# Optimization experiments

Hardware: AMD Instinct MI355X
Metric: run time of the kernel (lower is better)

Reference implementation:

```python
import jax, jax.numpy as jnp
import numpy as np

N_HEAD = 20
ALIGN_HEAD_IDX = (4, 7, 11)  # heads of alignment_heads with layer_idx == layer_index (2)


def setup_inputs() -> dict:
    key = jax.random.key(0)
    ks = jax.random.split(key, 7)
    B, Tq, Tk, D = 8, 448, 1500, 1280
    s = 1.0 / np.sqrt(D)
    return {
        "x": jax.random.normal(ks[0], (B, Tq, D), jnp.float32),
        "k": jax.random.normal(ks[1], (B, Tk, D), jnp.float32),
        "v": jax.random.normal(ks[2], (B, Tk, D), jnp.float32),
        "Wq": jax.random.normal(ks[3], (D, D), jnp.float32) * s,
        "bq": jax.random.normal(ks[4], (D,), jnp.float32) * 0.02,
        "Wo": jax.random.normal(ks[5], (D, D), jnp.float32) * s,
        "bo": jax.random.normal(ks[6], (D,), jnp.float32) * 0.02,
    }


def reference(x, k, v, Wq, bq, Wo, bo):
    B, Tq, D = x.shape
    H = N_HEAD
    Dh = D // H
    scale = Dh ** (-0.25)

    # q projection (torch Linear: x @ W.T + b)
    q = x @ Wq.T + bq                                   # [B, Tq, D]
    qh = q.reshape(B, Tq, H, Dh).transpose(0, 2, 1, 3)  # [B, H, Tq, Dh]
    kh = k.reshape(B, -1, H, Dh).transpose(0, 2, 1, 3)  # [B, H, Tk, Dh]
    vh = v.reshape(B, -1, H, Dh).transpose(0, 2, 1, 3)  # [B, H, Tk, Dh]

    # scaled QK^T, softmax in fp32
    qk = jnp.einsum("bhqd,bhkd->bhqk", qh * scale, kh * scale)
    w = jax.nn.softmax(qk.astype(jnp.float32), axis=-1).astype(q.dtype)

    out = jnp.einsum("bhqk,bhkd->bhqd", w, vh)          # [B, H, Tq, Dh]
    out = out.transpose(0, 2, 1, 3).reshape(B, Tq, D)
    out = out @ Wo.T + bo

    alignment_weights = w[:, jnp.array(ALIGN_HEAD_IDX), :, :]  # [B, 3, Tq, Tk]
    return out, alignment_weights
```

## Files before the change

kernel.cpp:

```cpp
#include <hip/hip_runtime.h>
#include <stdint.h>


typedef short bf16x8 __attribute__((ext_vector_type(8)));
typedef float f32x4  __attribute__((ext_vector_type(4)));

#define VMCNT(n) asm volatile("s_waitcnt vmcnt(" #n ")" ::: "memory")

__device__ __forceinline__ unsigned short f2bf(float f) {
  union { float f; unsigned int u; } c; c.f = f;
  unsigned int u = c.u;
  unsigned int r = (u + 0x7FFFu + ((u >> 16) & 1u)) >> 16;
  return (unsigned short)r;
}

__device__ __forceinline__ float exp2_hw(float x) {
  float r;
  asm("v_exp_f32 %0, %1" : "=v"(r) : "v"(x));
  return r;
}

__device__ __forceinline__ void gld_lds16(const void* g, void* l) {
  __builtin_amdgcn_global_load_lds(
      (__attribute__((address_space(1))) void*)g,
      (__attribute__((address_space(3))) void*)l, 16, 0, 0);
}

__device__ __forceinline__ bf16x8 ldfrag(const void* base, int row, int c16) {
  return *reinterpret_cast<const bf16x8*>(
      reinterpret_cast<const char*>(base) + (row << 7) + (((c16 ^ (row & 7))) << 4));
}
__device__ __forceinline__ bf16x8 ldfragV(const void* base, int row, int c16) {
  return *reinterpret_cast<const bf16x8*>(
      reinterpret_cast<const char*>(base) + (row << 8) + (((c16 ^ (row & 15))) << 4));
}

__global__ __launch_bounds__(256) void prep_kernel(
    const float* __restrict__ x,  unsigned short* __restrict__ xb,
    const float* __restrict__ Wq, unsigned short* __restrict__ wqb,
    const float* __restrict__ Wo, unsigned short* __restrict__ wob,
    const float* __restrict__ k,  unsigned short* __restrict__ kb,
    const float* __restrict__ v,  unsigned short* __restrict__ vbt) {
  __shared__ float T[64][65];
  int blk = blockIdx.x;
  if (blk < 22680) {
    const float* src; unsigned short* dst;
    if (blk < 4480)       { src = x;  dst = xb; }
    else if (blk < 6080)  { src = Wq; dst = wqb; blk -= 4480; }
    else if (blk < 7680)  { src = Wo; dst = wob; blk -= 6080; }
    else                  { src = k;  dst = kb;  blk -= 7680; }
    long i = ((long)blk * 256 + threadIdx.x) * 4;
    float4 val = *reinterpret_cast<const float4*>(src + i);
    ushort4 o;
    o.x = f2bf(val.x); o.y = f2bf(val.y); o.z = f2bf(val.z); o.w = f2bf(val.w);
    *reinterpret_cast<ushort4*>(dst + i) = o;
    return;
  }
  blk -= 22680;
  const int kt = blk % 24; blk /= 24;
  const int h = blk % 20; const int b = blk / 20;
  const int tid = threadIdx.x;
  const int c  = tid & 63;
  const int r0 = tid >> 6;
#pragma unroll
  for (int r = 0; r < 16; ++r) {
    const int tk = r * 4 + r0;
    const int gtk = kt * 64 + tk;
    float val = 0.f;
    if (gtk < 1500) val = v[(size_t)(b * 1500 + gtk) * 1280 + h * 64 + c];
    T[tk][c] = val;
  }
  __syncthreads();
#pragma unroll
  for (int r = 0; r < 16; ++r) {
    const int d = r * 4 + r0;
    vbt[((size_t)(b * 20 + h) * 64 + d) * 1536 + kt * 64 + c] = f2bf(T[c][d]);
  }
}

template <int EPI>
__global__ __launch_bounds__(256) void gemm_bt(const unsigned short* __restrict__ A,
                                               const unsigned short* __restrict__ Bm,
                                               const float* __restrict__ bias,
                                               void* __restrict__ Cout,
                                               int M, int N, int K, float scale) {
  __shared__ __attribute__((aligned(16))) unsigned short As[128 * 64];
  __shared__ __attribute__((aligned(16))) unsigned short Bs[128 * 64];
  const int tid = threadIdx.x;
  const int w = tid >> 6, lane = tid & 63;
  const int l15 = lane & 15, l4 = lane >> 4;
  const int nBlk = N >> 7;
  const int cpx = gridDim.x >> 3;
  const int bid = (blockIdx.x & 7) * cpx + (blockIdx.x >> 3);
  const int bm = bid / nBlk, bn = bid % nBlk;
  const int m0 = bm << 7, n0 = bn << 7;
  const int wr = (w >> 1) << 6, wc = (w & 1) << 6;

  f32x4 acc[4][4] = {};

  const int nKt = K >> 6;
  for (int kt = 0; kt < nKt; ++kt) {
    const int koff = kt << 6;
#pragma unroll
    for (int r = 0; r < 4; ++r) {
      const int base = (((w << 2) + r) << 10);
      const int p = base + (lane << 4);
      const int row = p >> 7;
      const int cb = (p & 127) >> 1;
      gld_lds16(A  + ((size_t)(m0 + row) * K + koff + cb), (char*)As + base);
      gld_lds16(Bm + ((size_t)(n0 + row) * K + koff + cb), (char*)Bs + base);
    }
    __syncthreads();
#pragma unroll
    for (int kk = 0; kk < 64; kk += 32) {
      bf16x8 af[4], bfr[4];
#pragma unroll
      for (int mi = 0; mi < 4; ++mi)
        af[mi] = *reinterpret_cast<const bf16x8*>(&As[(wr + mi * 16 + l15) * 64 + kk + l4 * 8]);
#pragma unroll
      for (int ni = 0; ni < 4; ++ni)
        bfr[ni] = *reinterpret_cast<const bf16x8*>(&Bs[(wc + ni * 16 + l15) * 64 + kk + l4 * 8]);
#pragma unroll
      for (int mi = 0; mi < 4; ++mi)
#pragma unroll
        for (int ni = 0; ni < 4; ++ni)
          acc[mi][ni] = __builtin_amdgcn_mfma_f32_16x16x32_bf16(af[mi], bfr[ni], acc[mi][ni], 0, 0, 0);
    }
    __syncthreads();
  }
#pragma unroll
  for (int ni = 0; ni < 4; ++ni) {
    const int n = n0 + wc + ni * 16 + l15;
    const float bv = bias[n];
#pragma unroll
    for (int mi = 0; mi < 4; ++mi) {
#pragma unroll
      for (int i = 0; i < 4; ++i) {
        const int m = m0 + wr + mi * 16 + l4 * 4 + i;
        float vv = (acc[mi][ni][i] + bv) * scale;
        if (EPI == 0)
          ((unsigned short*)Cout)[(size_t)m * N + n] = f2bf(vv);
        else
          ((float*)Cout)[(size_t)m * N + n] = vv;
      }
    }
  }
}

__global__ __launch_bounds__(256, 2) void attn_kernel(const unsigned short* __restrict__ Qg,
                                                      const unsigned short* __restrict__ Kg,
                                                      const unsigned short* __restrict__ Vtg,
                                                      unsigned short* __restrict__ Og,
                                                      float* __restrict__ ML) {
  __shared__ __attribute__((aligned(16))) char smem[81920];
  char* const K0 = smem;
  char* const K1 = smem + 16384;
  char* const V0 = smem + 32768;
  char* const V1 = smem + 49152;
  char* const Pw = smem + 65536 + (threadIdx.x >> 6) * 4096;

  const int tid = threadIdx.x;
  const int w = tid >> 6, lane = tid & 63;
  const int l15 = lane & 15, l4 = lane >> 4;
  int bid = (blockIdx.x & 7) * 140 + (blockIdx.x >> 3);
  const int qt = bid % 7; bid /= 7;
  const int h = bid % 20; const int b = bid / 20;
  const int tq0 = qt << 6;

  const int srK = lane >> 3;
  const int scK = ((lane & 7) ^ srK) << 3;
  const int vr4 = lane >> 4;
  const size_t vbase = ((size_t)(b * 20 + h)) * 64 * 1536;

  bf16x8 qreg[4][2];
#pragma unroll
  for (int qg = 0; qg < 4; ++qg) {
    const unsigned short* qp =
        Qg + (size_t)(b * 448 + tq0 + qg * 16 + l15) * 1280 + h * 64 + l4 * 8;
    qreg[qg][0] = *reinterpret_cast<const bf16x8*>(qp);
    qreg[qg][1] = *reinterpret_cast<const bf16x8*>(qp + 32);
  }

  auto stage = [&](int k0, char* Kd, char* Vd) {
#pragma unroll
    for (int c = 0; c < 4; ++c) {
      const int ch = (w << 2) + c;
      int tk = k0 + ch * 8 + srK; if (tk > 1499) tk = 1499;
      gld_lds16(Kg + ((size_t)(b * 1500 + tk)) * 1280 + h * 64 + scK, Kd + ch * 1024);
    }
#pragma unroll
    for (int c = 0; c < 4; ++c) {
      const int ch = (w << 2) + c;
      const int d = (ch << 2) + vr4;
      const int col = ((lane & 15) ^ ((c << 2) + vr4)) << 3;
      gld_lds16(Vtg + vbase + (size_t)d * 1536 + k0 + col, Vd + ch * 1024);
    }
  };

  stage(0, K0, V0);
  VMCNT(0);
  __builtin_amdgcn_s_barrier();

  float l_p[4] = {0.f, 0.f, 0.f, 0.f};
  f32x4 o_acc[4][4] = {};

  for (int kt = 0; kt < 12; ++kt) {
    const int cur = kt & 1;
    const char* Kb = cur ? K1 : K0;
    const char* Vb = cur ? V1 : V0;

    if (kt < 11) {
      stage((kt + 1) << 7, cur ? K0 : K1, cur ? V0 : V1);
      VMCNT(8);
    } else {
      VMCNT(0);
    }
    __builtin_amdgcn_s_barrier();

    f32x4 s[2][4] = {};
    __builtin_amdgcn_s_setprio(1);
#pragma unroll
    for (int h2 = 0; h2 < 2; ++h2) {
      bf16x8 kf0 = ldfrag(Kb, (w << 5) + l15,      (h2 << 2) + l4);
      bf16x8 kf1 = ldfrag(Kb, (w << 5) + 16 + l15, (h2 << 2) + l4);
#pragma unroll
      for (int qg = 0; qg < 4; ++qg)
        s[0][qg] = __builtin_amdgcn_mfma_f32_16x16x32_bf16(kf0, qreg[qg][h2], s[0][qg], 0, 0, 0);
#pragma unroll
      for (int qg = 0; qg < 4; ++qg)
        s[1][qg] = __builtin_amdgcn_mfma_f32_16x16x32_bf16(kf1, qreg[qg][h2], s[1][qg], 0, 0, 0);
    }
    __builtin_amdgcn_s_setprio(0);

    if (kt == 11) {
#pragma unroll
      for (int kg = 0; kg < 2; ++kg)
#pragma unroll
        for (int i = 0; i < 4; ++i)
          if ((w << 5) + (kg << 4) + (l4 << 2) + i >= 92) {
#pragma unroll
            for (int qg = 0; qg < 4; ++qg) s[kg][qg][i] = -1e30f;
          }
    }

#pragma unroll
    for (int kg = 0; kg < 2; ++kg)
#pragma unroll
      for (int qg = 0; qg < 4; ++qg) {
#pragma unroll
        for (int i = 0; i < 4; ++i) {
          float e = exp2_hw(fmaf(s[kg][qg][i], 1.44269504f, -17.31234049f));
          s[kg][qg][i] = e;
          l_p[qg] += e;
        }
        unsigned int u0, u1;
        asm("v_cvt_pk_bf16_f32 %0, %1, %2" : "=v"(u0) : "v"(s[kg][qg][0]), "v"(s[kg][qg][1]));
        asm("v_cvt_pk_bf16_f32 %0, %1, %2" : "=v"(u1) : "v"(s[kg][qg][2]), "v"(s[kg][qg][3]));
        unsigned long long u01 = ((unsigned long long)u1 << 32) | u0;
        *reinterpret_cast<unsigned long long*>(
            Pw + (qg << 10) + (((kg << 1) + (l4 >> 1)) << 8) + (l15 << 4) + ((l4 & 1) << 3)) = u01;
      }

    __builtin_amdgcn_s_setprio(1);
    bf16x8 bv[4];
#pragma unroll
    for (int dg = 0; dg < 4; ++dg)
      bv[dg] = ldfragV(Vb, (dg << 4) + l15, (w << 2) + l4);
#pragma unroll
    for (int qg = 0; qg < 4; ++qg) {
      bf16x8 ap = *reinterpret_cast<const bf16x8*>(Pw + (qg << 10) + (lane << 4));
#pragma unroll
      for (int dg = 0; dg < 4; ++dg)
        o_acc[qg][dg] = __builtin_amdgcn_mfma_f32_16x16x32_bf16(ap, bv[dg], o_acc[qg][dg], 0, 0, 0);
    }
    __builtin_amdgcn_s_setprio(0);
    __builtin_amdgcn_s_barrier();
  }

#pragma unroll
  for (int qg = 0; qg < 4; ++qg)
#pragma unroll
    for (int dg = 0; dg < 4; ++dg)
      *reinterpret_cast<f32x4*>(smem + (w << 14) + (((qg << 2) + dg) << 10) + (lane << 4)) =
          o_acc[qg][dg];

  float* Lb = (float*)(smem + 65536);
  float lw[4];
#pragma unroll
  for (int qg = 0; qg < 4; ++qg) {
    float t = l_p[qg] + __shfl_xor(l_p[qg], 16);
    t += __shfl_xor(t, 32);
    lw[qg] = t;
  }
  if (l4 == 0) {
#pragma unroll
    for (int qg = 0; qg < 4; ++qg) Lb[(w << 6) + (qg << 4) + l15] = lw[qg];
  }
  __syncthreads();

  float ltot = 0.f;
#pragma unroll
  for (int w2 = 0; w2 < 4; ++w2) ltot += Lb[(w2 << 6) + (w << 4) + l15];
  const float rr = 1.f / ltot;
  float rinv4[4], lt4[4];
#pragma unroll
  for (int i = 0; i < 4; ++i) {
    rinv4[i] = __shfl(rr,   (l4 << 2) + i);
    lt4[i]   = __shfl(ltot, (l4 << 2) + i);
  }
#pragma unroll
  for (int dg = 0; dg < 4; ++dg) {
    f32x4 t = *reinterpret_cast<const f32x4*>(
        smem + (((w << 2) + dg) << 10) + (lane << 4));
#pragma unroll
    for (int w2 = 1; w2 < 4; ++w2)
      t += *reinterpret_cast<const f32x4*>(
          smem + (w2 << 14) + (((w << 2) + dg) << 10) + (lane << 4));
#pragma unroll
    for (int i = 0; i < 4; ++i)
      Og[(size_t)(b * 448 + tq0 + (w << 4) + (l4 << 2) + i) * 1280 + h * 64 + (dg << 4) + l15] =
          f2bf(t[i] * rinv4[i]);
  }
  if (l15 == 0) {
#pragma unroll
    for (int i = 0; i < 4; ++i) {
      size_t idx = (size_t)(b * 20 + h) * 448 + tq0 + (w << 4) + (l4 << 2) + i;
      ML[idx * 2]     = 12.0f;
      ML[idx * 2 + 1] = lt4[i];
    }
  }
}

__global__ __launch_bounds__(256) void weights_kernel(const unsigned short* __restrict__ Qg,
                                                      const unsigned short* __restrict__ Kg,
                                                      const float* __restrict__ ML,
                                                      float* __restrict__ Wout) {
  __shared__ __attribute__((aligned(16))) unsigned short Ks0[64 * 64];
  __shared__ __attribute__((aligned(16))) unsigned short Ks1[64 * 64];
  const int tid = threadIdx.x;
  const int w = tid >> 6, lane = tid & 63;
  const int l15 = lane & 15, l4 = lane >> 4;
  int bid = (blockIdx.x & 7) * 21 + (blockIdx.x >> 3);
  const int qt = bid % 7; bid /= 7;
  const int ha = bid % 3; const int b = bid / 3;
  const int h = (ha == 0) ? 4 : (ha == 1) ? 7 : 11;
  const int tq0 = qt << 6;

  const int srow = lane >> 3;
  const int scol = ((lane & 7) ^ srow) << 3;

  const unsigned short* qptr =
      Qg + (size_t)(b * 448 + tq0 + w * 16 + l15) * 1280 + h * 64 + l4 * 8;
  bf16x8 qreg[2];
  qreg[0] = *reinterpret_cast<const bf16x8*>(qptr);
  qreg[1] = *reinterpret_cast<const bf16x8*>(qptr + 32);

#pragma unroll
  for (int c = 0; c < 2; ++c) {
    const int ch = w * 2 + c;
    const int row = ch * 8 + srow;
    int tk = row; if (tk > 1499) tk = 1499;
    gld_lds16(Kg + ((size_t)(b * 1500 + tk) * 1280 + h * 64 + scol), (char*)Ks0 + ch * 1024);
  }
  VMCNT(0);
  __builtin_amdgcn_s_barrier();

  float m_r[4], rinv[4];
#pragma unroll
  for (int i = 0; i < 4; ++i) {
    size_t idx = (size_t)(b * 20 + h) * 448 + tq0 + w * 16 + l4 * 4 + i;
    m_r[i]  = ML[idx * 2];
    rinv[i] = 1.f / ML[idx * 2 + 1];
  }
  float* wbase = Wout + ((size_t)(b * 3 + ha) * 448 + tq0) * 1500;

  for (int kt = 0; kt < 24; ++kt) {
    const int cur = kt & 1;
    const unsigned short* Kb = cur ? Ks1 : Ks0;
    unsigned short* Kn = cur ? Ks0 : Ks1;
    if (kt < 23) {
      const int k0n = (kt + 1) << 6;
#pragma unroll
      for (int c = 0; c < 2; ++c) {
        const int ch = w * 2 + c;
        const int row = ch * 8 + srow;
        int tk = k0n + row; if (tk > 1499) tk = 1499;
        gld_lds16(Kg + ((size_t)(b * 1500 + tk) * 1280 + h * 64 + scol), (char*)Kn + ch * 1024);
      }
      VMCNT(2);
    } else {
      VMCNT(0);
    }
    __builtin_amdgcn_s_barrier();

    f32x4 s[4] = {};
    __builtin_amdgcn_s_setprio(1);
#pragma unroll
    for (int h2 = 0; h2 < 2; ++h2) {
#pragma unroll
      for (int ni = 0; ni < 4; ++ni) {
        bf16x8 bk = ldfrag(Kb, ni * 16 + l15, h2 * 4 + l4);
        s[ni] = __builtin_amdgcn_mfma_f32_16x16x32_bf16(qreg[h2], bk, s[ni], 0, 0, 0);
      }
    }
    __builtin_amdgcn_s_setprio(0);

    const int k0 = kt << 6;
#pragma unroll
    for (int ni = 0; ni < 4; ++ni) {
      const int col = k0 + ni * 16 + l15;
      if (col < 1500) {
#pragma unroll
        for (int i = 0; i < 4; ++i) {
          const int row = w * 16 + l4 * 4 + i;
          wbase[(size_t)row * 1500 + col] = __expf(s[ni][i] - m_r[i]) * rinv[i];
        }
      }
    }
    __builtin_amdgcn_s_barrier();
  }
}

extern "C" void kernel_launch(void* const* d_in, const int* in_sizes, int n_in,
                              void* d_out, int out_size, void* d_ws, size_t ws_size,
                              hipStream_t stream) {
  const float* x  = (const float*)d_in[0];
  const float* k  = (const float*)d_in[1];
  const float* v  = (const float*)d_in[2];
  const float* Wq = (const float*)d_in[3];
  const float* bq = (const float*)d_in[4];
  const float* Wo = (const float*)d_in[5];
  const float* bo = (const float*)d_in[6];
  float* out  = (float*)d_out;
  float* wout = out + (size_t)8 * 448 * 1280;

  char* ws = (char*)d_ws;
  unsigned short* xb  = (unsigned short*)(ws);
  unsigned short* wqb = (unsigned short*)(ws + 9175040);
  unsigned short* wob = (unsigned short*)(ws + 12451840);
  unsigned short* kb  = (unsigned short*)(ws + 15728640);
  unsigned short* vbt = (unsigned short*)(ws + 46448640);
  unsigned short* qs  = (unsigned short*)(ws + 77905920);
  unsigned short* ao  = (unsigned short*)(ws + 87080960);
  float* ml           = (float*)(ws + 96256000);

  prep_kernel<<<26520, 256, 0, stream>>>(x, xb, Wq, wqb, Wo, wob, k, kb, v, vbt);

  gemm_bt<0><<<280, 256, 0, stream>>>(xb, wqb, bq, (void*)qs, 3584, 1280, 1280, 0.125f);

  attn_kernel<<<8 * 20 * 7, 256, 0, stream>>>(qs, kb, vbt, ao, ml);

  gemm_bt<1><<<280, 256, 0, stream>>>(ao, wob, bo, (void*)out, 3584, 1280, 1280, 1.0f);

  weights_kernel<<<8 * 3 * 7, 256, 0, stream>>>(qs, kb, ml, wout);
}
```

Baseline: 188.3 us.

## Double-buffer GEMM tiles and split prep into vectorized convert and V-transpose kernels

The GEMM now keeps two LDS buffers per operand and issues the global-to-LDS loads for the next K tile before computing the current one. It waits with vmcnt and raw barriers instead of __syncthreads, and raises wave priority around the MFMA block, so load latency overlaps compute. The fp32-to-bf16 preprocessing is split into a grid-stride convert kernel that handles 8 elements per thread with wider stores, relying on the destination buffers being contiguous in the workspace. A separate V transpose kernel works on 128-row tiles, converts to bf16 before writing to swizzled LDS, and emits 16-byte stores. The cost is doubled GEMM LDS (64KB), which may lower occupancy, plus an extra kernel launch.

```diff
diff --git a/kernel.cpp b/kernel.cpp
--- a/kernel.cpp
+++ b/kernel.cpp
@@ -35,46 +35,73 @@
       reinterpret_cast<const char*>(base) + (row << 8) + (((c16 ^ (row & 15))) << 4));
 }
 
-__global__ __launch_bounds__(256) void prep_kernel(
-    const float* __restrict__ x,  unsigned short* __restrict__ xb,
-    const float* __restrict__ Wq, unsigned short* __restrict__ wqb,
-    const float* __restrict__ Wo, unsigned short* __restrict__ wob,
-    const float* __restrict__ k,  unsigned short* __restrict__ kb,
-    const float* __restrict__ v,  unsigned short* __restrict__ vbt) {
-  __shared__ float T[64][65];
+__global__ __launch_bounds__(256) void cvt_kernel(const float* __restrict__ s0,
+                                                  const float* __restrict__ s1,
+                                                  const float* __restrict__ s2,
+                                                  const float* __restrict__ s3,
+                                                  unsigned short* __restrict__ dst) {
+  const int n0 = 573440, n1 = 204800, n2 = 204800;
+  const int total = 2903040;
+  for (int i = blockIdx.x * 256 + threadIdx.x; i < total; i += gridDim.x * 256) {
+    const float* src; int j = i;
+    if (j < n0)               { src = s0; }
+    else if ((j -= n0) < n1)  { src = s1; }
+    else if ((j -= n1) < n2)  { src = s2; }
+    else                      { j -= n2; src = s3; }
+    float4 a = *reinterpret_cast<const float4*>(src + (size_t)j * 8);
+    float4 b = *reinterpret_cast<const float4*>(src + (size_t)j * 8 + 4);
+    uint4 o;
+    o.x = f2bf(a.x) | ((unsigned int)f2bf(a.y) << 16);
+    o.y = f2bf(a.z) | ((unsigned int)f2bf(a.w) << 16);
+    o.z = f2bf(b.x) | ((unsigned int)f2bf(b.y) << 16);
+    o.w = f2bf(b.z) | ((unsigned int)f2bf(b.w) << 16);
+    *reinterpret_cast<uint4*>(dst + (size_t)i * 8) = o;
+  }
+}
+
+__global__ __launch_bounds__(256) void vt_kernel(const float* __restrict__ v,
+                                                 unsigned short* __restrict__ vbt) {
+  __shared__ __attribute__((aligned(16))) char T[128 * 132];
   int blk = blockIdx.x;
-  if (blk < 22680) {
-    const float* src; unsigned short* dst;
-    if (blk < 4480)       { src = x;  dst = xb; }
-    else if (blk < 6080)  { src = Wq; dst = wqb; blk -= 4480; }
-    else if (blk < 7680)  { src = Wo; dst = wob; blk -= 6080; }
-    else                  { src = k;  dst = kb;  blk -= 7680; }
-    long i = ((long)blk * 256 + threadIdx.x) * 4;
-    float4 val = *reinterpret_cast<const float4*>(src + i);
-    ushort4 o;
-    o.x = f2bf(val.x); o.y = f2bf(val.y); o.z = f2bf(val.z); o.w = f2bf(val.w);
-    *reinterpret_cast<ushort4*>(dst + i) = o;
-    return;
-  }
-  blk -= 22680;
-  const int kt = blk % 24; blk /= 24;
+  const int kt = blk % 12; blk /= 12;
   const int h = blk % 20; const int b = blk / 20;
-  const int tid = threadIdx.x;
-  const int c  = tid & 63;
-  const int r0 = tid >> 6;
-#pragma unroll
-  for (int r = 0; r < 16; ++r) {
-    const int tk = r * 4 + r0;
-    const int gtk = kt * 64 + tk;
-    float val = 0.f;
-    if (gtk < 1500) val = v[(size_t)(b * 1500 + gtk) * 1280 + h * 64 + c];
-    T[tk][c] = val;
+  const int t = threadIdx.x;
+
+  const int c4 = t & 15;
+  const int r  = t >> 4;
+#pragma unroll
+  for (int p = 0; p < 8; ++p) {
+    const int k = p * 16 + r;
+    const int gtk = kt * 128 + k;
+    float4 a = {0.f, 0.f, 0.f, 0.f};
+    if (gtk < 1500)
+      a = *reinterpret_cast<const float4*>(v + (size_t)(b * 1500 + gtk) * 1280 + h * 64 + c4 * 4);
+    unsigned int lo = f2bf(a.x) | ((unsigned int)f2bf(a.y) << 16);
+    unsigned int hi = f2bf(a.z) | ((unsigned int)f2bf(a.w) << 16);
+    char* base = T + k * 132 + ((c4 ^ (k & 15)) << 3);
+    *reinterpret_cast<unsigned int*>(base)     = lo;
+    *reinterpret_cast<unsigned int*>(base + 4) = hi;
   }
   __syncthreads();
-#pragma unroll
-  for (int r = 0; r < 16; ++r) {
-    const int d = r * 4 + r0;
-    vbt[((size_t)(b * 20 + h) * 64 + d) * 1536 + kt * 64 + c] = f2bf(T[c][d]);
+
+  const int kc = t & 15;
+#pragma unroll
+  for (int p = 0; p < 4; ++p) {
+    const int d = p * 16 + (t >> 4);
+    unsigned short r8[8];
+#pragma unroll
+    for (int j = 0; j < 8; ++j) {
+      const int k = kc * 8 + j;
+      r8[j] = *reinterpret_cast<const unsigned short*>(
+          T + k * 132 + (((d >> 2) ^ (k & 15)) << 3) + ((d & 3) << 1));
+    }
+    uint4 o;
+    o.x = r8[0] | ((unsigned int)r8[1] << 16);
+    o.y = r8[2] | ((unsigned int)r8[3] << 16);
+    o.z = r8[4] | ((unsigned int)r8[5] << 16);
+    o.w = r8[6] | ((unsigned int)r8[7] << 16);
+    *reinterpret_cast<uint4*>(
+        vbt + ((size_t)((b * 20 + h) * 64 + d)) * 1536 + kt * 128 + kc * 8) = o;
   }
 }
 
@@ -84,8 +111,8 @@
                                                const float* __restrict__ bias,
                                                void* __restrict__ Cout,
                                                int M, int N, int K, float scale) {
-  __shared__ __attribute__((aligned(16))) unsigned short As[128 * 64];
-  __shared__ __attribute__((aligned(16))) unsigned short Bs[128 * 64];
+  __shared__ __attribute__((aligned(16))) unsigned short As[2][128 * 64];
+  __shared__ __attribute__((aligned(16))) unsigned short Bs[2][128 * 64];
   const int tid = threadIdx.x;
   const int w = tid >> 6, lane = tid & 63;
   const int l15 = lane & 15, l4 = lane >> 4;
@@ -98,8 +125,7 @@
 
   f32x4 acc[4][4] = {};
 
-  const int nKt = K >> 6;
-  for (int kt = 0; kt < nKt; ++kt) {
+  auto stage = [&](int kt, int buf) {
     const int koff = kt << 6;
 #pragma unroll
     for (int r = 0; r < 4; ++r) {
@@ -107,27 +133,46 @@
       const int p = base + (lane << 4);
       const int row = p >> 7;
       const int cb = (p & 127) >> 1;
-      gld_lds16(A  + ((size_t)(m0 + row) * K + koff + cb), (char*)As + base);
-      gld_lds16(Bm + ((size_t)(n0 + row) * K + koff + cb), (char*)Bs + base);
-    }
-    __syncthreads();
+      gld_lds16(A  + ((size_t)(m0 + row) * K + koff + cb), (char*)As[buf] + base);
+      gld_lds16(Bm + ((size_t)(n0 + row) * K + koff + cb), (char*)Bs[buf] + base);
+    }
+  };
+
+  const int nKt = K >> 6;
+  stage(0, 0);
+  VMCNT(0);
+  __builtin_amdgcn_s_barrier();
+
+  for (int kt = 0; kt < nKt; ++kt) {
+    const int buf = kt & 1;
+    if (kt + 1 < nKt) {
+      stage(kt + 1, buf ^ 1);
+      VMCNT(8);
+    } else {
+      VMCNT(0);
+    }
+    __builtin_amdgcn_s_barrier();
+
+    __builtin_amdgcn_s_setprio(1);
 #pragma unroll
     for (int kk = 0; kk < 64; kk += 32) {
       bf16x8 af[4], bfr[4];
 #pragma unroll
       for (int mi = 0; mi < 4; ++mi)
-        af[mi] = *reinterpret_cast<const bf16x8*>(&As[(wr + mi * 16 + l15) * 64 + kk + l4 * 8]);
+        af[mi] = *reinterpret_cast<const bf16x8*>(&As[buf][(wr + mi * 16 + l15) * 64 + kk + l4 * 8]);
 #pragma unroll
       for (int ni = 0; ni < 4; ++ni)
-        bfr[ni] = *reinterpret_cast<const bf16x8*>(&Bs[(wc + ni * 16 + l15) * 64 + kk + l4 * 8]);
+        bfr[ni] = *reinterpret_cast<const bf16x8*>(&Bs[buf][(wc + ni * 16 + l15) * 64 + kk + l4 * 8]);
 #pragma unroll
       for (int mi = 0; mi < 4; ++mi)
 #pragma unroll
         for (int ni = 0; ni < 4; ++ni)
           acc[mi][ni] = __builtin_amdgcn_mfma_f32_16x16x32_bf16(af[mi], bfr[ni], acc[mi][ni], 0, 0, 0);
     }
-    __syncthreads();
-  }
+    __builtin_amdgcn_s_setprio(0);
+    __builtin_amdgcn_s_barrier();
+  }
+
 #pragma unroll
   for (int ni = 0; ni < 4; ++ni) {
     const int n = n0 + wc + ni * 16 + l15;
@@ -444,7 +489,8 @@
   unsigned short* ao  = (unsigned short*)(ws + 87080960);
   float* ml           = (float*)(ws + 96256000);
 
-  prep_kernel<<<26520, 256, 0, stream>>>(x, xb, Wq, wqb, Wo, wob, k, kb, v, vbt);
+  cvt_kernel<<<2048, 256, 0, stream>>>(x, Wq, Wo, k, xb);
+  vt_kernel<<<1920, 256, 0, stream>>>(v, vbt);
 
   gemm_bt<0><<<280, 256, 0, stream>>>(xb, wqb, bq, (void*)qs, 3584, 1280, 1280, 0.125f);
 
```

Result: no change. 189.4 us (+0.6%).
